# Kernel tuning notes

Measured on AMD Instinct MI355X. Metric: run time of the kernel, lower is better.

Reference implementation:

```python
import jax, jax.numpy as jnp
import numpy as np

EPS_DIV = 1e-7   # matches .div(sigma + 1e-07) and denominator + 1e-07
EPS_NORM = 1e-12  # torch F.normalize default eps


def setup_inputs() -> dict:
    key = jax.random.key(0)
    k1, k2, k3, k4 = jax.random.split(key, 4)
    B, C, H, W = 4, 128, 64, 64
    K = 32
    stdv = 1.0 / np.sqrt(C)
    return {
        "x": jax.random.normal(k1, (B, C, H, W), dtype=jnp.float32),
        "anchor": jax.random.uniform(k2, (K, C), dtype=jnp.float32),
        "sigma_param": jax.random.uniform(k3, (K, C), dtype=jnp.float32),
        "gcn_weight": jax.random.uniform(k4, (C, C), dtype=jnp.float32,
                                         minval=-stdv, maxval=stdv),
    }


def _l2_normalize(v, axis):
    n = jnp.sqrt(jnp.sum(v * v, axis=axis, keepdims=True))
    return v / jnp.maximum(n, EPS_NORM)


def reference(x, anchor, sigma_param, gcn_weight):
    B, C, H, W = x.shape
    N = H * W
    K = anchor.shape[0]

    # --- GraphNet (NetVLAD-style soft assignment pooling) ---
    sigma = jax.nn.sigmoid(sigma_param)                        # [K, C]
    xf = x.reshape(B, C, N).transpose(0, 2, 1)                 # [B, N, C]
    # residual: [B, K, N, C]
    residual = (xf[:, None, :, :] - anchor[None, :, None, :]) / (
        sigma[None, :, None, :] + EPS_DIV)
    logits = -0.5 * jnp.sum(residual * residual, axis=3)       # [B, K, N]
    soft_assign = jax.nn.softmax(logits, axis=1)               # softmax over nodes K

    numerator = jnp.einsum('bknc,bkn->bkc', residual, soft_assign)  # [B, K, C]
    denominator = jnp.sum(soft_assign, axis=2)[..., None]           # [B, K, 1]
    nodes = numerator / (denominator + EPS_DIV)                     # [B, K, C]

    nodes = _l2_normalize(nodes, axis=2)
    flat = nodes.reshape(B, -1)
    flat = _l2_normalize(flat, axis=1)
    graph = flat.reshape(B, C, K)  # note: pure reshape as in torch .view

    # --- CascadeGCNet, loop = 1 ---
    adj = jnp.einsum('bck,bcl->bkl', graph, graph)             # x_t @ x -> [B, K, K]
    adj = jax.nn.softmax(adj, axis=2)
    support = jnp.einsum('bck,cd->bkd', graph, gcn_weight)     # [B, K, C]
    graph = jnp.einsum('bkl,bld->bkd', adj, support).transpose(0, 2, 1)  # [B, C, K]
    graph = jax.nn.relu(graph)

    # --- project back ---
    out = jnp.einsum('bck,bkn->bcn', graph, soft_assign)       # [B, C, N]
    return out.reshape(B, C, H, W)
```

## Files before the change

kernel.cpp:

```cpp
#include <hip/hip_runtime.h>
#include <math.h>

#define BB 4
#define CC 128
#define KK 32
#define NN 4096
#define NSL 64

__launch_bounds__(1024, 4)
__global__ void k_A(const float* __restrict__ x, const float* __restrict__ anchor,
                    const float* __restrict__ sigp, float* __restrict__ sa,
                    float* __restrict__ pnum, float* __restrict__ pden) {
  const int b  = blockIdx.y, s = blockIdx.x;
  const int n0 = s * 64;
  const int t  = threadIdx.x;
  const int lane = t & 63;
  const int w  = __builtin_amdgcn_readfirstlane(t >> 6);

  __shared__ float4 wt4[16][129];
  __shared__ float  lgT[64][36];
  __shared__ float  stK[KK][68];
  __shared__ float  ckL[KK];
  __shared__ float  pdenP[8][36];

  {
    const int kp = w;
    const int k0 = kp * 2, k1 = k0 + 1;
    float s0 = 0.f, s1 = 0.f;
#pragma unroll
    for (int e = 0; e < 2; e++) {
      int c = lane * 2 + e;
      float sp0 = sigp[k0 * CC + c], sp1 = sigp[k1 * CC + c];
      float a0  = anchor[k0 * CC + c], a1 = anchor[k1 * CC + c];
      float sg0 = 1.0f / (1.0f + expf(-sp0));
      float sg1 = 1.0f / (1.0f + expf(-sp1));
      float iv0 = 1.0f / (sg0 + 1e-7f), iv1 = 1.0f / (sg1 + 1e-7f);
      float w20 = iv0 * iv0, w21 = iv1 * iv1;
      wt4[kp][c] = make_float4(w20, -2.0f * a0 * w20, w21, -2.0f * a1 * w21);
      s0 = fmaf(a0 * a0, w20, s0);
      s1 = fmaf(a1 * a1, w21, s1);
    }
#pragma unroll
    for (int d = 1; d < 64; d <<= 1) {
      s0 += __shfl_xor(s0, d);
      s1 += __shfl_xor(s1, d);
    }
    if (lane == 0) { ckL[k0] = s0; ckL[k1] = s1; }
  }
  __syncthreads();

  {
    const int p = lane, kp = w;
    float l0 = 0.f, l1 = 0.f;
    const float* xp = x + (size_t)b * CC * NN + n0 + p;
    for (int c = 0; c < CC; c++) {
      float xv = xp[(size_t)c * NN];
      float4 wv = wt4[kp][c];
      l0 = fmaf(xv, fmaf(xv, wv.x, wv.y), l0);
      l1 = fmaf(xv, fmaf(xv, wv.z, wv.w), l1);
    }
    *(float2*)&lgT[p][kp * 2] = make_float2(l0, l1);
  }
  __syncthreads();

  if (t < 512) {
    const int p  = w * 8 + (lane >> 3);
    const int kq = lane & 7;
    float4 lg  = *(float4*)&lgT[p][kq * 4];
    float4 ckv = *(float4*)&ckL[kq * 4];
    float4 lv;
    lv.x = -0.5f * (lg.x + ckv.x);
    lv.y = -0.5f * (lg.y + ckv.y);
    lv.z = -0.5f * (lg.z + ckv.z);
    lv.w = -0.5f * (lg.w + ckv.w);
    float m = fmaxf(fmaxf(lv.x, lv.y), fmaxf(lv.z, lv.w));
    m = fmaxf(m, __shfl_xor(m, 1));
    m = fmaxf(m, __shfl_xor(m, 2));
    m = fmaxf(m, __shfl_xor(m, 4));
    float e0 = __expf(lv.x - m), e1 = __expf(lv.y - m);
    float e2 = __expf(lv.z - m), e3 = __expf(lv.w - m);
    float sum = e0 + e1 + e2 + e3;
    sum += __shfl_xor(sum, 1);
    sum += __shfl_xor(sum, 2);
    sum += __shfl_xor(sum, 4);
    float rs = 1.0f / sum;
    e0 *= rs; e1 *= rs; e2 *= rs; e3 *= rs;
    stK[kq * 4 + 0][p] = e0;
    stK[kq * 4 + 1][p] = e1;
    stK[kq * 4 + 2][p] = e2;
    stK[kq * 4 + 3][p] = e3;
    float p0 = e0, p1 = e1, p2 = e2, p3 = e3;
    p0 += __shfl_xor(p0, 8);  p1 += __shfl_xor(p1, 8);
    p2 += __shfl_xor(p2, 8);  p3 += __shfl_xor(p3, 8);
    p0 += __shfl_xor(p0, 16); p1 += __shfl_xor(p1, 16);
    p2 += __shfl_xor(p2, 16); p3 += __shfl_xor(p3, 16);
    p0 += __shfl_xor(p0, 32); p1 += __shfl_xor(p1, 32);
    p2 += __shfl_xor(p2, 32); p3 += __shfl_xor(p3, 32);
    if (lane < 8) {
      pdenP[w][lane * 4 + 0] = p0;
      pdenP[w][lane * 4 + 1] = p1;
      pdenP[w][lane * 4 + 2] = p2;
      pdenP[w][lane * 4 + 3] = p3;
    }
  }
  __syncthreads();

  if (t < KK) {
    float d = 0.f;
#pragma unroll
    for (int ww = 0; ww < 8; ww++) d += pdenP[ww][t];
    pden[((size_t)b * NSL + s) * KK + t] = d;
  }

  if (t < 512) {
    const int k = t >> 4, j4 = t & 15;
    float4 v = *(float4*)&stK[k][4 * j4];
    *(float4*)(sa + ((size_t)b * KK + k) * NN + n0 + 4 * j4) = v;
  }

  {
    const int k = t & 31, cg = t >> 5;
    float acc[4];
#pragma unroll
    for (int i = 0; i < 4; i++) acc[i] = 0.f;
    const float* xb = x + (size_t)(b * CC + cg * 4) * NN + n0;
    for (int j4 = 0; j4 < 16; j4++) {
      float4 sv = *(float4*)&stK[k][4 * j4];
#pragma unroll
      for (int i = 0; i < 4; i++) {
        float4 xr = *(const float4*)(xb + (size_t)i * NN + 4 * j4);
        acc[i] = fmaf(sv.x, xr.x, acc[i]);
        acc[i] = fmaf(sv.y, xr.y, acc[i]);
        acc[i] = fmaf(sv.z, xr.z, acc[i]);
        acc[i] = fmaf(sv.w, xr.w, acc[i]);
      }
    }
    float* pp = pnum + (((size_t)b * NSL + s) * KK + k) * CC + cg * 4;
    *(float4*)pp = make_float4(acc[0], acc[1], acc[2], acc[3]);
  }
}

__launch_bounds__(256)
__global__ void k_red(const float* __restrict__ pnum, const float* __restrict__ pden,
                      const float* __restrict__ sigp, const float* __restrict__ anchor,
                      float* __restrict__ nodes, float* __restrict__ n1sq) {
  const int t = threadIdx.x;
  const int g = blockIdx.x * 256 + t;
  const int c = g & 127, k = (g >> 7) & 31, b = g >> 12;

  float dk = 0.0f;
#pragma unroll 8
  for (int s = 0; s < NSL; s++) dk += pden[((size_t)b * NSL + s) * KK + k];

  float q = 0.0f;
#pragma unroll 8
  for (int s = 0; s < NSL; s++)
    q += pnum[(((size_t)b * NSL + s) * KK + k) * CC + c];

  const int idx = k * CC + c;
  float sg = 1.0f / (1.0f + expf(-sigp[idx]));
  float iv = 1.0f / (sg + 1e-7f);
  float val = iv * (q - anchor[idx] * dk) / (dk + 1e-7f);
  nodes[((size_t)b * KK + k) * CC + c] = val;

  __shared__ float red[256];
  red[t] = val * val;
  __syncthreads();
  for (int sft = 64; sft > 0; sft >>= 1) {
    if ((t & 127) < sft) red[t] += red[t + sft];
    __syncthreads();
  }
  if ((t & 127) == 0) n1sq[b * KK + k] = red[t];
}

__launch_bounds__(1024)
__global__ void k_gcn2(const float* __restrict__ nodes, const float* __restrict__ n1sq,
                       const float* __restrict__ W, float* __restrict__ GB) {
  const int b = blockIdx.x;
  const int t = threadIdx.x;
  __shared__ float flat[KK * CC];
  __shared__ float sup[KK][130];
  __shared__ float adjm[KK][33];
  __shared__ float n1v[KK], nsq[KK];
  __shared__ float n2s;

  const int k = t >> 5, cq = t & 31;
  float4 val = ((const float4*)(nodes + (size_t)b * KK * CC))[k * 32 + cq];

  if (t < KK) {
    float s2 = n1sq[b * KK + t];
    float n1 = fmaxf(sqrtf(s2), 1e-12f);
    n1v[t] = n1;
    nsq[t] = s2 / (n1 * n1);
  }
  __syncthreads();
  if (t == 0) {
    float tot = 0.0f;
#pragma unroll
    for (int kk = 0; kk < KK; kk++) tot += nsq[kk];
    n2s = fmaxf(sqrtf(tot), 1e-12f);
  }
  __syncthreads();
  {
    float sc = 1.0f / (n1v[k] * n2s);
    val.x *= sc; val.y *= sc; val.z *= sc; val.w *= sc;
    ((float4*)flat)[k * 32 + cq] = val;
  }
  __syncthreads();

  {
    const int k2 = t >> 5, l = t & 31;
    float a = 0.0f;
#pragma unroll 8
    for (int i = 0; i < CC; i++)
      a = fmaf(flat[i * KK + k2], flat[i * KK + l], a);
    adjm[k2][l] = a;
  }
  __syncthreads();
  if (t < KK) {
    float m = -1e30f;
#pragma unroll
    for (int l = 0; l < KK; l++) m = fmaxf(m, adjm[t][l]);
    float s2 = 0.0f;
#pragma unroll
    for (int l = 0; l < KK; l++) { float e = __expf(adjm[t][l] - m); adjm[t][l] = e; s2 += e; }
    float r = 1.0f / s2;
#pragma unroll
    for (int l = 0; l < KK; l++) adjm[t][l] *= r;
  }
  __syncthreads();

  const int d = t & 127, lg = t >> 7;
  float sacc[4] = {0.0f, 0.0f, 0.0f, 0.0f};
  for (int c = 0; c < CC; c++) {
    float wv = W[c * CC + d];
#pragma unroll
    for (int j = 0; j < 4; j++)
      sacc[j] = fmaf(flat[c * KK + lg + 8 * j], wv, sacc[j]);
  }
#pragma unroll
  for (int j = 0; j < 4; j++) sup[lg + 8 * j][d] = sacc[j];
  __syncthreads();

#pragma unroll
  for (int j = 0; j < 4; j++) {
    int kk = lg + 8 * j;
    float g = 0.0f;
#pragma unroll
    for (int l = 0; l < KK; l++) g = fmaf(adjm[kk][l], sup[l][d], g);
    GB[((size_t)b * CC + d) * KK + kk] = fmaxf(g, 0.0f);
  }
}

__launch_bounds__(256)
__global__ void k_proj(const float* __restrict__ GB, const float* __restrict__ sa,
                       float* __restrict__ out) {
  const int b  = blockIdx.z, cqt = blockIdx.y;
  const int n0 = blockIdx.x * 64;
  const int t  = threadIdx.x;
  const int nl = t & 63;
  const int cg = __builtin_amdgcn_readfirstlane(t >> 6);
  const int c0 = cqt * 32 + cg * 8;

  float sreg[KK];
  const float* spt = sa + (size_t)b * KK * NN + n0 + nl;
#pragma unroll
  for (int k = 0; k < KK; k++) sreg[k] = spt[(size_t)k * NN];

  const float* gp = GB + ((size_t)b * CC + c0) * KK;
  float* op = out + ((size_t)b * CC + c0) * NN + n0 + nl;
#pragma unroll
  for (int ci = 0; ci < 8; ci++) {
    float acc = 0.0f;
#pragma unroll
    for (int k = 0; k < KK; k++) acc = fmaf(gp[ci * KK + k], sreg[k], acc);
    op[(size_t)ci * NN] = acc;
  }
}

extern "C" void kernel_launch(void* const* d_in, const int* in_sizes, int n_in,
                              void* d_out, int out_size, void* d_ws, size_t ws_size,
                              hipStream_t stream) {
  const float* x      = (const float*)d_in[0];
  const float* anchor = (const float*)d_in[1];
  const float* sigp   = (const float*)d_in[2];
  const float* W      = (const float*)d_in[3];
  float* out = (float*)d_out;

  float* ws    = (float*)d_ws;
  float* pden  = ws;
  float* pnum  = ws + 8192;
  float* nodes = ws + 1056768;
  float* n1sq  = ws + 1073152;
  float* GB    = ws + 1073280;
  float* sa    = ws + 1089664;

  k_A   <<<dim3(NSL, BB),     dim3(1024), 0, stream>>>(x, anchor, sigp, sa, pnum, pden);
  k_red <<<dim3(64),          dim3(256),  0, stream>>>(pnum, pden, sigp, anchor, nodes, n1sq);
  k_gcn2<<<dim3(BB),          dim3(1024), 0, stream>>>(nodes, n1sq, W, GB);
  k_proj<<<dim3(64, 4, BB),   dim3(256),  0, stream>>>(GB, sa, out);
}
```

Measured before the change: 59.74 us.

## Fuse GCN and projection kernels with redundant per-slice GCN; stage x tile in LDS

Merges the GCN kernel, which ran only 4 blocks, with the projection kernel into one kernel of 256 blocks. Each block recomputes the small per-batch GCN (adjacency, support, relu) in shared memory and then projects its 64-pixel slice, removing one launch and the GB round trip through global memory. In k_A the x tile is now loaded into LDS with float4 loads, and logits are computed with a 4-pixel by 4-channel-chunk register tiling before the partials are summed. The cost is 64x redundant GCN work per batch, including repeated reads of the W matrix, plus more LDS use that may reduce occupancy.

```diff
diff --git a/kernel.cpp b/kernel.cpp
--- a/kernel.cpp
+++ b/kernel.cpp
@@ -17,11 +17,22 @@
   const int lane = t & 63;
   const int w  = __builtin_amdgcn_readfirstlane(t >> 6);
 
+  __shared__ float  xt[CC][68];
   __shared__ float4 wt4[16][129];
-  __shared__ float  lgT[64][36];
+  __shared__ float  plg[4][64][36];
   __shared__ float  stK[KK][68];
   __shared__ float  ckL[KK];
   __shared__ float  pdenP[8][36];
+
+  {
+#pragma unroll
+    for (int e = 0; e < 2; e++) {
+      int i = t + e * 1024;
+      int c = i >> 4, pq = i & 15;
+      float4 v = *(const float4*)(x + ((size_t)b * CC + c) * NN + n0 + 4 * pq);
+      *(float4*)&xt[c][4 * pq] = v;
+    }
+  }
 
   {
     const int kp = w;
@@ -50,29 +61,42 @@
   __syncthreads();
 
   {
-    const int p = lane, kp = w;
-    float l0 = 0.f, l1 = 0.f;
-    const float* xp = x + (size_t)b * CC * NN + n0 + p;
-    for (int c = 0; c < CC; c++) {
-      float xv = xp[(size_t)c * NN];
+    const int px4 = t & 15, kp = (t >> 4) & 15, ch = t >> 8;
+    float acc[4][2];
+#pragma unroll
+    for (int i = 0; i < 4; i++) { acc[i][0] = 0.f; acc[i][1] = 0.f; }
+    for (int c0 = 0; c0 < 32; c0++) {
+      const int c = ch * 32 + c0;
+      float4 xv = *(const float4*)&xt[c][px4 * 4];
       float4 wv = wt4[kp][c];
-      l0 = fmaf(xv, fmaf(xv, wv.x, wv.y), l0);
-      l1 = fmaf(xv, fmaf(xv, wv.z, wv.w), l1);
-    }
-    *(float2*)&lgT[p][kp * 2] = make_float2(l0, l1);
+#pragma unroll
+      for (int i = 0; i < 4; i++) {
+        float xs = (&xv.x)[i];
+        acc[i][0] = fmaf(xs, fmaf(xs, wv.x, wv.y), acc[i][0]);
+        acc[i][1] = fmaf(xs, fmaf(xs, wv.z, wv.w), acc[i][1]);
+      }
+    }
+#pragma unroll
+    for (int i = 0; i < 4; i++) {
+      plg[ch][px4 * 4 + i][kp * 2 + 0] = acc[i][0];
+      plg[ch][px4 * 4 + i][kp * 2 + 1] = acc[i][1];
+    }
   }
   __syncthreads();
 
   if (t < 512) {
     const int p  = w * 8 + (lane >> 3);
     const int kq = lane & 7;
-    float4 lg  = *(float4*)&lgT[p][kq * 4];
+    float4 l0  = *(float4*)&plg[0][p][kq * 4];
+    float4 l1  = *(float4*)&plg[1][p][kq * 4];
+    float4 l2  = *(float4*)&plg[2][p][kq * 4];
+    float4 l3  = *(float4*)&plg[3][p][kq * 4];
     float4 ckv = *(float4*)&ckL[kq * 4];
     float4 lv;
-    lv.x = -0.5f * (lg.x + ckv.x);
-    lv.y = -0.5f * (lg.y + ckv.y);
-    lv.z = -0.5f * (lg.z + ckv.z);
-    lv.w = -0.5f * (lg.w + ckv.w);
+    lv.x = -0.5f * (l0.x + l1.x + l2.x + l3.x + ckv.x);
+    lv.y = -0.5f * (l0.y + l1.y + l2.y + l3.y + ckv.y);
+    lv.z = -0.5f * (l0.z + l1.z + l2.z + l3.z + ckv.z);
+    lv.w = -0.5f * (l0.w + l1.w + l2.w + l3.w + ckv.w);
     float m = fmaxf(fmaxf(lv.x, lv.y), fmaxf(lv.z, lv.w));
     m = fmaxf(m, __shfl_xor(m, 1));
     m = fmaxf(m, __shfl_xor(m, 2));
@@ -173,14 +197,17 @@
   if ((t & 127) == 0) n1sq[b * KK + k] = red[t];
 }
 
-__launch_bounds__(1024)
-__global__ void k_gcn2(const float* __restrict__ nodes, const float* __restrict__ n1sq,
-                       const float* __restrict__ W, float* __restrict__ GB) {
-  const int b = blockIdx.x;
+__launch_bounds__(1024, 4)
+__global__ void k_BC(const float* __restrict__ nodes, const float* __restrict__ n1sq,
+                     const float* __restrict__ W, const float* __restrict__ sa,
+                     float* __restrict__ out) {
+  const int b = blockIdx.y, s = blockIdx.x;
+  const int n0 = s * 64;
   const int t = threadIdx.x;
   __shared__ float flat[KK * CC];
   __shared__ float sup[KK][130];
   __shared__ float adjm[KK][33];
+  __shared__ float gbL[CC][KK + 1];
   __shared__ float n1v[KK], nsq[KK];
   __shared__ float n2s;
 
@@ -230,51 +257,50 @@
   }
   __syncthreads();
 
-  const int d = t & 127, lg = t >> 7;
-  float sacc[4] = {0.0f, 0.0f, 0.0f, 0.0f};
-  for (int c = 0; c < CC; c++) {
-    float wv = W[c * CC + d];
-#pragma unroll
-    for (int j = 0; j < 4; j++)
-      sacc[j] = fmaf(flat[c * KK + lg + 8 * j], wv, sacc[j]);
-  }
-#pragma unroll
-  for (int j = 0; j < 4; j++) sup[lg + 8 * j][d] = sacc[j];
-  __syncthreads();
-
-#pragma unroll
-  for (int j = 0; j < 4; j++) {
-    int kk = lg + 8 * j;
-    float g = 0.0f;
-#pragma unroll
-    for (int l = 0; l < KK; l++) g = fmaf(adjm[kk][l], sup[l][d], g);
-    GB[((size_t)b * CC + d) * KK + kk] = fmaxf(g, 0.0f);
-  }
-}
-
-__launch_bounds__(256)
-__global__ void k_proj(const float* __restrict__ GB, const float* __restrict__ sa,
-                       float* __restrict__ out) {
-  const int b  = blockIdx.z, cqt = blockIdx.y;
-  const int n0 = blockIdx.x * 64;
-  const int t  = threadIdx.x;
-  const int nl = t & 63;
-  const int cg = __builtin_amdgcn_readfirstlane(t >> 6);
-  const int c0 = cqt * 32 + cg * 8;
-
-  float sreg[KK];
-  const float* spt = sa + (size_t)b * KK * NN + n0 + nl;
-#pragma unroll
-  for (int k = 0; k < KK; k++) sreg[k] = spt[(size_t)k * NN];
-
-  const float* gp = GB + ((size_t)b * CC + c0) * KK;
-  float* op = out + ((size_t)b * CC + c0) * NN + n0 + nl;
-#pragma unroll
-  for (int ci = 0; ci < 8; ci++) {
-    float acc = 0.0f;
-#pragma unroll
-    for (int k = 0; k < KK; k++) acc = fmaf(gp[ci * KK + k], sreg[k], acc);
-    op[(size_t)ci * NN] = acc;
+  {
+    const int d = t & 127, lg = t >> 7;
+    float sacc[4] = {0.0f, 0.0f, 0.0f, 0.0f};
+    for (int c = 0; c < CC; c++) {
+      float wv = W[c * CC + d];
+#pragma unroll
+      for (int j = 0; j < 4; j++)
+        sacc[j] = fmaf(flat[c * KK + lg + 8 * j], wv, sacc[j]);
+    }
+#pragma unroll
+    for (int j = 0; j < 4; j++) sup[lg + 8 * j][d] = sacc[j];
+  }
+  __syncthreads();
+
+  {
+    const int d = t & 127, lg = t >> 7;
+#pragma unroll
+    for (int j = 0; j < 4; j++) {
+      int kk = lg + 8 * j;
+      float g = 0.0f;
+#pragma unroll
+      for (int l = 0; l < KK; l++) g = fmaf(adjm[kk][l], sup[l][d], g);
+      gbL[d][kk] = fmaxf(g, 0.0f);
+    }
+  }
+  __syncthreads();
+
+  {
+    const int nl = t & 63, cw = t >> 6;
+    const int c0 = cw * 8;
+    float sreg[KK];
+    const float* spt = sa + (size_t)b * KK * NN + n0 + nl;
+#pragma unroll
+    for (int kk = 0; kk < KK; kk++) sreg[kk] = spt[(size_t)kk * NN];
+
+    float* op = out + ((size_t)b * CC + c0) * NN + n0 + nl;
+#pragma unroll
+    for (int ci = 0; ci < 8; ci++) {
+      float acc = 0.0f;
+#pragma unroll
+      for (int kk = 0; kk < KK; kk++)
+        acc = fmaf(gbL[c0 + ci][kk], sreg[kk], acc);
+      op[(size_t)ci * NN] = acc;
+    }
   }
 }
 
@@ -292,11 +318,9 @@
   float* pnum  = ws + 8192;
   float* nodes = ws + 1056768;
   float* n1sq  = ws + 1073152;
-  float* GB    = ws + 1073280;
-  float* sa    = ws + 1089664;
-
-  k_A   <<<dim3(NSL, BB),     dim3(1024), 0, stream>>>(x, anchor, sigp, sa, pnum, pden);
-  k_red <<<dim3(64),          dim3(256),  0, stream>>>(pnum, pden, sigp, anchor, nodes, n1sq);
-  k_gcn2<<<dim3(BB),          dim3(1024), 0, stream>>>(nodes, n1sq, W, GB);
-  k_proj<<<dim3(64, 4, BB),   dim3(256),  0, stream>>>(GB, sa, out);
+  float* sa    = ws + 1073280;
+
+  k_A  <<<dim3(NSL, BB), dim3(1024), 0, stream>>>(x, anchor, sigp, sa, pnum, pden);
+  k_red<<<dim3(64),      dim3(256),  0, stream>>>(pnum, pden, sigp, anchor, nodes, n1sq);
+  k_BC <<<dim3(NSL, BB), dim3(1024), 0, stream>>>(nodes, n1sq, W, sa, out);
 }
```

After: 54.29 us (median of 3 runs). 1.1x faster.
